# Kernel tuning notes

Measured on AMD Instinct MI355X. Metric: run time of the kernel, lower is better.

The kernel has to match this reference:

```python
import jax, jax.numpy as jnp
import numpy as np

EMBED = 8192      # DYNAMIC(2048) + STATIC(6144)
U0, U1 = 1024, 256  # units
EGO = 3
NUM_HEAD = 6
ACTION = 2
MEAN_SCALE = 5.0
INIT_STD = 5.0
MIN_STD = 1e-4
BATCH = 8192


def setup_inputs() -> dict:
    key = jax.random.key(0)
    ks = jax.random.split(key, 10)
    s = lambda fan_in: 1.0 / np.sqrt(fan_in)
    x = jax.random.normal(ks[0], (BATCH, EMBED), dtype=jnp.float32)
    # command head index in [0, 6) == RoadOption.value - 1
    command = jax.random.randint(ks[1], (BATCH,), 0, NUM_HEAD, dtype=jnp.int32)
    ego_state = jax.random.normal(ks[2], (BATCH, EGO), dtype=jnp.float32)
    # shared trunk fc: Linear(EMBED -> U0)
    fc_W = jax.random.uniform(ks[3], (EMBED, U0), jnp.float32, -s(EMBED), s(EMBED))
    fc_b = jax.random.uniform(ks[4], (U0,), jnp.float32, -s(EMBED), s(EMBED))
    # per-head MLP: Linear(U0+EGO -> U1) -> ReLU -> Linear(U1 -> 2*ACTION)
    cin = U0 + EGO
    W1 = jax.random.uniform(ks[5], (NUM_HEAD, cin, U1), jnp.float32, -s(cin), s(cin))
    b1 = jax.random.uniform(ks[6], (NUM_HEAD, U1), jnp.float32, -s(cin), s(cin))
    W2 = jax.random.uniform(ks[7], (NUM_HEAD, U1, 2 * ACTION), jnp.float32, -s(U1), s(U1))
    b2 = jax.random.uniform(ks[8], (NUM_HEAD, 2 * ACTION), jnp.float32, -s(U1), s(U1))
    return {"x": x, "command": command, "ego_state": ego_state,
            "fc_W": fc_W, "fc_b": fc_b, "W1": W1, "b1": b1, "W2": W2, "b2": b2}


def reference(x, command, ego_state, fc_W, fc_b, W1, b1, W2, b2):
    # shared trunk: Linear + ReLU, then concat ego state -> [B, U0+EGO]
    h = jax.nn.relu(x @ fc_W + fc_b)
    h = jnp.concatenate([h, ego_state], axis=-1)
    # routed heads: compute all 6 small heads densely, then select per sample
    # (faithful math; an optimized kernel would gather->grouped GEMM->scatter)
    h1 = jax.nn.relu(jnp.einsum('bi,hio->bho', h, W1) + b1)          # [B, H, U1]
    h2 = jnp.einsum('bhi,hio->bho', h1, W2) + b2                      # [B, H, 2A]
    sel = jnp.take_along_axis(h2, command[:, None, None].astype(jnp.int32), axis=1)
    out = sel[:, 0, :]                                                # [B, 2A]
    mean, std = jnp.split(out, 2, axis=-1)
    mean = MEAN_SCALE * jnp.tanh(mean / MEAN_SCALE)
    raw_init_std = np.float32(np.log(np.exp(INIT_STD) - 1.0))
    std = jax.nn.softplus(std + raw_init_std) + MIN_STD
    # distribution parameters (pre TanhBijector Normal params)
    return jnp.concatenate([mean, std], axis=-1)
```

## Files before the change

kernel.cpp:

```cpp
#include <hip/hip_runtime.h>
#include <stdint.h>

typedef short bf16x8 __attribute__((ext_vector_type(8)));
typedef float f32x4 __attribute__((ext_vector_type(4)));

#define BATCH 8192
#define EMBED 8192
#define U0    1024
#define U1    256
#define NHEAD 6

__device__ __forceinline__ unsigned short f2bf(float f) {
  union { float f; unsigned int u; } v; v.f = f;
  unsigned int u = v.u;
  unsigned int r = u + 0x7FFFu + ((u >> 16) & 1u);
  return (unsigned short)(r >> 16);
}
__device__ __forceinline__ unsigned int pk2(float lo, float hi) {
  return (unsigned int)f2bf(lo) | ((unsigned int)f2bf(hi) << 16);
}
__device__ __forceinline__ void async_copy16(const void* g, void* l) {
  __builtin_amdgcn_global_load_lds((const __attribute__((address_space(1))) void*)g,
                                   (__attribute__((address_space(3))) void*)l, 16, 0, 0);
}

__global__ void cvt_x_kernel(const float* __restrict__ x, unsigned short* __restrict__ xb) {
  long i = ((long)blockIdx.x * 256 + threadIdx.x) * 8;
  float4 a = *(const float4*)(x + i);
  float4 b = *(const float4*)(x + i + 4);
  uint4 r;
  r.x = pk2(a.x, a.y); r.y = pk2(a.z, a.w);
  r.z = pk2(b.x, b.y); r.w = pk2(b.z, b.w);
  *(uint4*)(xb + i) = r;
}

__global__ void transpose_cvt_kernel(const float* __restrict__ in, unsigned short* __restrict__ out,
                                     int R, int C, long in_z, long out_z) {
  __shared__ unsigned short tile[64][65];
  const float* inp = in + (long)blockIdx.z * in_z;
  unsigned short* outp = out + (long)blockIdx.z * out_z;
  int r0 = blockIdx.x * 64;
  int c0 = blockIdx.y * 64;
  int lc = threadIdx.x & 63;
  int lr = threadIdx.x >> 6;
#pragma unroll
  for (int i = 0; i < 16; i++) {
    int r = lr + i * 4;
    tile[r][lc] = f2bf(inp[(long)(r0 + r) * C + (c0 + lc)]);
  }
  __syncthreads();
#pragma unroll
  for (int i = 0; i < 16; i++) {
    int c = lr + i * 4;
    outp[(long)(c0 + c) * R + (r0 + lc)] = tile[lc][c];
  }
}

__global__ void bucket_kernel(const int* __restrict__ cmd, int* __restrict__ idxlist,
                              int* __restrict__ meta) {
  __shared__ int cnt[NHEAD], cur[NHEAD], off[NHEAD + 1];
  int tid = threadIdx.x;
  if (tid < NHEAD) cnt[tid] = 0;
  __syncthreads();
  for (int b = tid; b < BATCH; b += blockDim.x) atomicAdd(&cnt[cmd[b]], 1);
  __syncthreads();
  if (tid == 0) {
    int s = 0;
    for (int h2 = 0; h2 < NHEAD; h2++) { off[h2] = s; s += cnt[h2]; }
    off[NHEAD] = s;
  }
  __syncthreads();
  if (tid < NHEAD) cur[tid] = off[tid];
  if (tid <= NHEAD) meta[tid] = off[tid];
  __syncthreads();
  for (int b = tid; b < BATCH; b += blockDim.x) {
    int p = atomicAdd(&cur[cmd[b]], 1);
    idxlist[p] = b;
  }
}

__global__ __launch_bounds__(256) void gemm_kernel(const unsigned short* __restrict__ xb,
                                                   const unsigned short* __restrict__ wt,
                                                   const float* __restrict__ fc_b,
                                                   unsigned short* __restrict__ h) {
  __shared__ uint4 As[1024];
  __shared__ uint4 Bs[1024];
  int tid  = threadIdx.x;
  int lane = tid & 63;
  int wave = tid >> 6;
  int wm = wave >> 1, wn = wave & 1;
  int m0 = blockIdx.y * 128;
  int n0 = blockIdx.x * 128;
  int l15 = lane & 15, lq = lane >> 4;

  long asrc[4], bsrc[4];
#pragma unroll
  for (int j = 0; j < 4; j++) {
    int c = wave * 4 + j;
    int cwm = c >> 3, cks = (c >> 2) & 1, cmi = c & 3;
    int kofs = cks * 32 + lq * 8;
    asrc[j] = (long)(m0 + cwm * 64 + cmi * 16 + l15) * EMBED + kofs;
    bsrc[j] = (long)(n0 + cwm * 64 + cmi * 16 + l15) * EMBED + kofs;
  }

  f32x4 zero = {0.f, 0.f, 0.f, 0.f};
  f32x4 acc[4][4];
#pragma unroll
  for (int mi = 0; mi < 4; mi++)
#pragma unroll
    for (int ni = 0; ni < 4; ni++) acc[mi][ni] = zero;

  for (int k0 = 0; k0 < EMBED; k0 += 64) {
    __syncthreads();
#pragma unroll
    for (int j = 0; j < 4; j++) {
      int c = wave * 4 + j;
      async_copy16(xb + asrc[j] + k0, &As[c * 64 + lane]);
      async_copy16(wt + bsrc[j] + k0, &Bs[c * 64 + lane]);
    }
    __syncthreads();
#pragma unroll
    for (int ks = 0; ks < 2; ks++) {
      bf16x8 af[4], bfr[4];
#pragma unroll
      for (int mi = 0; mi < 4; mi++) af[mi] = *(const bf16x8*)&As[((wm * 2 + ks) * 4 + mi) * 64 + lane];
#pragma unroll
      for (int ni = 0; ni < 4; ni++) bfr[ni] = *(const bf16x8*)&Bs[((wn * 2 + ks) * 4 + ni) * 64 + lane];
#pragma unroll
      for (int mi = 0; mi < 4; mi++)
#pragma unroll
        for (int ni = 0; ni < 4; ni++)
          acc[mi][ni] = __builtin_amdgcn_mfma_f32_16x16x32_bf16(af[mi], bfr[ni], acc[mi][ni], 0, 0, 0);
    }
  }

#pragma unroll
  for (int ni = 0; ni < 4; ni++) {
    int col = n0 + wn * 64 + ni * 16 + l15;
    float bias = fc_b[col];
#pragma unroll
    for (int mi = 0; mi < 4; mi++) {
      int rbase = m0 + wm * 64 + mi * 16 + lq * 4;
#pragma unroll
      for (int r = 0; r < 4; r++) {
        float v = acc[mi][ni][r] + bias;
        v = v > 0.f ? v : 0.f;
        h[(long)(rbase + r) * U0 + col] = f2bf(v);
      }
    }
  }
}

__global__ __launch_bounds__(256) void head_kernel(const unsigned short* __restrict__ h,
                                                   const unsigned short* __restrict__ w1t,
                                                   const float* __restrict__ W1,
                                                   const float* __restrict__ b1,
                                                   const float* __restrict__ W2,
                                                   const float* __restrict__ b2,
                                                   const float* __restrict__ ego,
                                                   const int* __restrict__ idxlist,
                                                   const int* __restrict__ meta,
                                                   float* __restrict__ out) {
  int hd = blockIdx.y;
  int off = meta[hd];
  int cnt = meta[hd + 1] - off;
  int t0 = blockIdx.x * 32;
  if (t0 >= cnt) return;

  __shared__ int ridx[32];
  __shared__ float h1s[32][257];
  int tid = threadIdx.x;
  if (tid < 32) {
    int i = t0 + tid;
    ridx[tid] = idxlist[off + (i < cnt ? i : 0)];
  }
  __syncthreads();

  int lane = tid & 63, wave = tid >> 6;
  int l15 = lane & 15, lq = lane >> 4;

  long abase[2];
#pragma unroll
  for (int mi = 0; mi < 2; mi++) abase[mi] = (long)ridx[mi * 16 + l15] * U0 + lq * 8;
  long bbase[4];
#pragma unroll
  for (int ni = 0; ni < 4; ni++)
    bbase[ni] = (long)(hd * 256 + wave * 64 + ni * 16 + l15) * 1024 + lq * 8;

  f32x4 zero = {0.f, 0.f, 0.f, 0.f};
  f32x4 acc[2][4];
#pragma unroll
  for (int mi = 0; mi < 2; mi++)
#pragma unroll
    for (int ni = 0; ni < 4; ni++) acc[mi][ni] = zero;

#pragma unroll 2
  for (int k0 = 0; k0 < 1024; k0 += 32) {
    bf16x8 af[2], bfr[4];
#pragma unroll
    for (int mi = 0; mi < 2; mi++) af[mi] = *(const bf16x8*)(h + abase[mi] + k0);
#pragma unroll
    for (int ni = 0; ni < 4; ni++) bfr[ni] = *(const bf16x8*)(w1t + bbase[ni] + k0);
#pragma unroll
    for (int mi = 0; mi < 2; mi++)
#pragma unroll
      for (int ni = 0; ni < 4; ni++)
        acc[mi][ni] = __builtin_amdgcn_mfma_f32_16x16x32_bf16(af[mi], bfr[ni], acc[mi][ni], 0, 0, 0);
  }

  const float* W1e = W1 + (long)hd * 1027 * 256 + (long)1024 * 256;
#pragma unroll
  for (int mi = 0; mi < 2; mi++)
#pragma unroll
    for (int r = 0; r < 4; r++) {
      int rl = mi * 16 + lq * 4 + r;
      int b = ridx[rl];
      float e0 = ego[b * 3 + 0], e1 = ego[b * 3 + 1], e2 = ego[b * 3 + 2];
#pragma unroll
      for (int ni = 0; ni < 4; ni++) {
        int col = wave * 64 + ni * 16 + l15;
        float v = acc[mi][ni][r] + b1[hd * 256 + col]
                + e0 * W1e[col] + e1 * W1e[256 + col] + e2 * W1e[512 + col];
        h1s[rl][col] = v > 0.f ? v : 0.f;
      }
    }
  __syncthreads();

  if (tid < 128) {
    int t = tid >> 2, o2 = tid & 3;
    if (t0 + t < cnt) {
      const float* w2 = W2 + (long)hd * 256 * 4;
      float sum = b2[hd * 4 + o2];
      for (int i = 0; i < 256; i++) sum += h1s[t][i] * w2[i * 4 + o2];
      int b = ridx[t];
      float res;
      if (o2 < 2) {
        res = 5.0f * tanhf(sum * 0.2f);
      } else {
        float z = sum + 4.99323838f;
        res = (z > 20.f ? z : log1pf(expf(z))) + 1e-4f;
      }
      out[b * 4 + o2] = res;
    }
  }
}

extern "C" void kernel_launch(void* const* d_in, const int* in_sizes, int n_in,
                              void* d_out, int out_size, void* d_ws, size_t ws_size,
                              hipStream_t stream) {
  const float* x   = (const float*)d_in[0];
  const int*   cmd = (const int*)d_in[1];
  const float* ego = (const float*)d_in[2];
  const float* fcW = (const float*)d_in[3];
  const float* fcb = (const float*)d_in[4];
  const float* W1  = (const float*)d_in[5];
  const float* b1  = (const float*)d_in[6];
  const float* W2  = (const float*)d_in[7];
  const float* b2  = (const float*)d_in[8];
  float* out = (float*)d_out;

  char* ws = (char*)d_ws;
  unsigned short* xb   = (unsigned short*)(ws);
  unsigned short* wt   = (unsigned short*)(ws + 134217728);
  unsigned short* hbuf = (unsigned short*)(ws + 150994944);
  unsigned short* w1t  = (unsigned short*)(ws + 167772160);
  int* idxlist         = (int*)(ws + 170917888);
  int* meta            = (int*)(ws + 170950656);

  hipLaunchKernelGGL(cvt_x_kernel, dim3(32768), dim3(256), 0, stream, x, xb);
  hipLaunchKernelGGL(transpose_cvt_kernel, dim3(128, 16, 1), dim3(256), 0, stream,
                     fcW, wt, 8192, 1024, 0L, 0L);
  hipLaunchKernelGGL(transpose_cvt_kernel, dim3(16, 4, 6), dim3(256), 0, stream,
                     W1, w1t, 1024, 256, (long)1027 * 256, (long)256 * 1024);
  hipLaunchKernelGGL(bucket_kernel, dim3(1), dim3(1024), 0, stream, cmd, idxlist, meta);
  hipLaunchKernelGGL(gemm_kernel, dim3(8, 64), dim3(256), 0, stream, xb, wt, fcb, hbuf);
  hipLaunchKernelGGL(head_kernel, dim3(256, 6), dim3(256), 0, stream,
                     hbuf, w1t, W1, b1, W2, b2, ego, idxlist, meta, out);
}
```

Measured before the change: 757.2 us.

## Parallelize bucketing with wave ballots and deepen GEMM K-tile to 128

The single-block bucket kernel becomes a 32-block kernel that uses wave ballots plus one global atomic per wave, writing each head's indices into its own fixed BATCH-sized slot so no prefix sum is needed. The head counters are zeroed inside the conversion kernel. The trunk GEMM now stages 128-wide K tiles (double the LDS), which halves the number of barrier pairs. Its grid is also swapped so consecutive blocks walk M while sharing an N tile. Index order within a head becomes nondeterministic, and the larger LDS footprint may lower occupancy.

```diff
diff --git a/kernel.cpp b/kernel.cpp
--- a/kernel.cpp
+++ b/kernel.cpp
@@ -24,7 +24,9 @@
                                    (__attribute__((address_space(3))) void*)l, 16, 0, 0);
 }
 
-__global__ void cvt_x_kernel(const float* __restrict__ x, unsigned short* __restrict__ xb) {
+__global__ void cvt_x_kernel(const float* __restrict__ x, unsigned short* __restrict__ xb,
+                             int* __restrict__ meta) {
+  if (blockIdx.x == 0 && threadIdx.x < 8) meta[threadIdx.x] = 0;
   long i = ((long)blockIdx.x * 256 + threadIdx.x) * 8;
   float4 a = *(const float4*)(x + i);
   float4 b = *(const float4*)(x + i + 4);
@@ -58,24 +60,17 @@
 
 __global__ void bucket_kernel(const int* __restrict__ cmd, int* __restrict__ idxlist,
                               int* __restrict__ meta) {
-  __shared__ int cnt[NHEAD], cur[NHEAD], off[NHEAD + 1];
-  int tid = threadIdx.x;
-  if (tid < NHEAD) cnt[tid] = 0;
-  __syncthreads();
-  for (int b = tid; b < BATCH; b += blockDim.x) atomicAdd(&cnt[cmd[b]], 1);
-  __syncthreads();
-  if (tid == 0) {
-    int s = 0;
-    for (int h2 = 0; h2 < NHEAD; h2++) { off[h2] = s; s += cnt[h2]; }
-    off[NHEAD] = s;
-  }
-  __syncthreads();
-  if (tid < NHEAD) cur[tid] = off[tid];
-  if (tid <= NHEAD) meta[tid] = off[tid];
-  __syncthreads();
-  for (int b = tid; b < BATCH; b += blockDim.x) {
-    int p = atomicAdd(&cur[cmd[b]], 1);
-    idxlist[p] = b;
+  int b = blockIdx.x * 256 + threadIdx.x;
+  int lane = threadIdx.x & 63;
+  int c = cmd[b];
+#pragma unroll
+  for (int h2 = 0; h2 < NHEAD; h2++) {
+    unsigned long long m = __ballot(c == h2);
+    int mypos = __popcll(m & ((1ull << lane) - 1ull));
+    int base = 0;
+    if (lane == 0 && m) base = atomicAdd(&meta[h2], __popcll(m));
+    base = __shfl(base, 0);
+    if (c == h2) idxlist[h2 * BATCH + base + mypos] = b;
   }
 }
 
@@ -83,25 +78,19 @@
                                                    const unsigned short* __restrict__ wt,
                                                    const float* __restrict__ fc_b,
                                                    unsigned short* __restrict__ h) {
-  __shared__ uint4 As[1024];
-  __shared__ uint4 Bs[1024];
+  __shared__ uint4 As[2048];
+  __shared__ uint4 Bs[2048];
   int tid  = threadIdx.x;
   int lane = tid & 63;
   int wave = tid >> 6;
   int wm = wave >> 1, wn = wave & 1;
-  int m0 = blockIdx.y * 128;
-  int n0 = blockIdx.x * 128;
+  int m0 = blockIdx.x * 128;
+  int n0 = blockIdx.y * 128;
   int l15 = lane & 15, lq = lane >> 4;
 
-  long asrc[4], bsrc[4];
-#pragma unroll
-  for (int j = 0; j < 4; j++) {
-    int c = wave * 4 + j;
-    int cwm = c >> 3, cks = (c >> 2) & 1, cmi = c & 3;
-    int kofs = cks * 32 + lq * 8;
-    asrc[j] = (long)(m0 + cwm * 64 + cmi * 16 + l15) * EMBED + kofs;
-    bsrc[j] = (long)(n0 + cwm * 64 + cmi * 16 + l15) * EMBED + kofs;
-  }
+  long abase = (long)(m0 + (wave >> 1) * 64 + l15) * EMBED + (wave & 1) * 64 + lq * 8;
+  long bbase = (long)(n0 + (wave >> 1) * 64 + l15) * EMBED + (wave & 1) * 64 + lq * 8;
+  int slbase = wave * 8 * 64 + lane;
 
   f32x4 zero = {0.f, 0.f, 0.f, 0.f};
   f32x4 acc[4][4];
@@ -110,22 +99,22 @@
 #pragma unroll
     for (int ni = 0; ni < 4; ni++) acc[mi][ni] = zero;
 
-  for (int k0 = 0; k0 < EMBED; k0 += 64) {
+  for (int k0 = 0; k0 < EMBED; k0 += 128) {
     __syncthreads();
 #pragma unroll
-    for (int j = 0; j < 4; j++) {
-      int c = wave * 4 + j;
-      async_copy16(xb + asrc[j] + k0, &As[c * 64 + lane]);
-      async_copy16(wt + bsrc[j] + k0, &Bs[c * 64 + lane]);
+    for (int j = 0; j < 8; j++) {
+      long ofs = (long)(j & 3) * 16 * EMBED + (j >> 2) * 32 + k0;
+      async_copy16(xb + abase + ofs, &As[slbase + j * 64]);
+      async_copy16(wt + bbase + ofs, &Bs[slbase + j * 64]);
     }
     __syncthreads();
 #pragma unroll
-    for (int ks = 0; ks < 2; ks++) {
+    for (int ks = 0; ks < 4; ks++) {
       bf16x8 af[4], bfr[4];
 #pragma unroll
-      for (int mi = 0; mi < 4; mi++) af[mi] = *(const bf16x8*)&As[((wm * 2 + ks) * 4 + mi) * 64 + lane];
-#pragma unroll
-      for (int ni = 0; ni < 4; ni++) bfr[ni] = *(const bf16x8*)&Bs[((wn * 2 + ks) * 4 + ni) * 64 + lane];
+      for (int mi = 0; mi < 4; mi++) af[mi] = *(const bf16x8*)&As[((wm * 4 + ks) * 4 + mi) * 64 + lane];
+#pragma unroll
+      for (int ni = 0; ni < 4; ni++) bfr[ni] = *(const bf16x8*)&Bs[((wn * 4 + ks) * 4 + ni) * 64 + lane];
 #pragma unroll
       for (int mi = 0; mi < 4; mi++)
 #pragma unroll
@@ -162,8 +151,8 @@
                                                    const int* __restrict__ meta,
                                                    float* __restrict__ out) {
   int hd = blockIdx.y;
-  int off = meta[hd];
-  int cnt = meta[hd + 1] - off;
+  int cnt = meta[hd];
+  int off = hd * BATCH;
   int t0 = blockIdx.x * 32;
   if (t0 >= cnt) return;
 
@@ -265,15 +254,15 @@
   unsigned short* hbuf = (unsigned short*)(ws + 150994944);
   unsigned short* w1t  = (unsigned short*)(ws + 167772160);
   int* idxlist         = (int*)(ws + 170917888);
-  int* meta            = (int*)(ws + 170950656);
-
-  hipLaunchKernelGGL(cvt_x_kernel, dim3(32768), dim3(256), 0, stream, x, xb);
+  int* meta            = (int*)(ws + 171114496);
+
+  hipLaunchKernelGGL(cvt_x_kernel, dim3(32768), dim3(256), 0, stream, x, xb, meta);
   hipLaunchKernelGGL(transpose_cvt_kernel, dim3(128, 16, 1), dim3(256), 0, stream,
                      fcW, wt, 8192, 1024, 0L, 0L);
   hipLaunchKernelGGL(transpose_cvt_kernel, dim3(16, 4, 6), dim3(256), 0, stream,
                      W1, w1t, 1024, 256, (long)1027 * 256, (long)256 * 1024);
-  hipLaunchKernelGGL(bucket_kernel, dim3(1), dim3(1024), 0, stream, cmd, idxlist, meta);
-  hipLaunchKernelGGL(gemm_kernel, dim3(8, 64), dim3(256), 0, stream, xb, wt, fcb, hbuf);
+  hipLaunchKernelGGL(bucket_kernel, dim3(32), dim3(256), 0, stream, cmd, idxlist, meta);
+  hipLaunchKernelGGL(gemm_kernel, dim3(64, 8), dim3(256), 0, stream, xb, wt, fcb, hbuf);
   hipLaunchKernelGGL(head_kernel, dim3(256, 6), dim3(256), 0, stream,
                      hbuf, w1t, W1, b1, W2, b2, ego, idxlist, meta, out);
 }
```

Result: slower. 829.6 us (+9.6%).
